# Performance work log

Measured on AMD Instinct MI355X. Metric: run time of the kernel, lower is better.

The kernel has to match this reference:

```python
import jax, jax.numpy as jnp
import numpy as np

B, N, C = 4, 4096, 256
H, D, K = 8, 32, 16  # heads, dim_head, knn


def setup_inputs() -> dict:
    key = jax.random.key(0)
    ks = jax.random.split(key, 7)
    s = 1.0 / np.sqrt(C)
    return {
        "x": jax.random.normal(ks[0], (B, N, C), dtype=jnp.float32),
        "Wq": jax.random.normal(ks[1], (C, H * D), dtype=jnp.float32) * s,
        "bq": jnp.zeros((H * D,), dtype=jnp.float32),
        "Wk": jax.random.normal(ks[2], (C, H * D), dtype=jnp.float32) * s,
        "bk": jnp.zeros((H * D,), dtype=jnp.float32),
        "Wv": jax.random.normal(ks[3], (C, H * D), dtype=jnp.float32) * s,
        "bv": jnp.zeros((H * D,), dtype=jnp.float32),
    }


def _knn_indices(x):
    # squared euclidean distances per batch: [B, N, N]
    sq = jnp.sum(x * x, axis=-1)
    d2 = sq[:, :, None] + sq[:, None, :] - 2.0 * jnp.einsum("bnc,bmc->bnm", x, x)
    # exclude self-loops (loop=False)
    eye = jnp.eye(x.shape[1], dtype=bool)
    d2 = jnp.where(eye[None], jnp.inf, d2)
    # k nearest neighbors (smallest distance)
    _, idx = jax.lax.top_k(-d2, K)  # [B, N, K]
    return idx


def reference(x, Wq, bq, Wk, bk, Wv, bv):
    idx = _knn_indices(x)  # [B, N, K] neighbor (source) node ids per target node
    # gather neighbor features: [B, N, K, C]
    xj = jax.vmap(lambda xb, ib: xb[ib])(x, idx)
    q = (x @ Wq + bq).reshape(B, N, H, D)           # target-node queries
    ke = (xj @ Wk + bk).reshape(B, N, K, H, D)      # per-edge keys
    ve = (xj @ Wv + bv).reshape(B, N, K, H, D)      # per-edge values
    scale = 1.0 / np.sqrt(D)
    scores = jnp.einsum("bnhd,bnkhd->bnkh", q, ke) * scale
    alpha = jax.nn.softmax(scores, axis=2)          # softmax over each node's K neighbors
    out = jnp.einsum("bnkh,bnkhd->bnhd", alpha, ve)
    return out.reshape(B, N, H * D)
```

## Files before the change

### kernel.cpp

```cpp
#include <hip/hip_runtime.h>
#include <cstdint>
#include <cstddef>

#define N_ 4096
#define C_ 256

typedef _Float16 h8 __attribute__((ext_vector_type(8)));
typedef _Float16 h4 __attribute__((ext_vector_type(4)));
typedef float f4 __attribute__((ext_vector_type(4)));

__device__ __forceinline__ void gl2lds16(const void* g, void* l) {
  __builtin_amdgcn_global_load_lds((const __attribute__((address_space(1))) void*)g,
                                   (__attribute__((address_space(3))) void*)l, 16, 0, 0);
}

__device__ __forceinline__ void ce_asc(double& a, double& b) {
  double mn = fmin(a, b), mx = fmax(a, b);
  a = mn; b = mx;
}

__device__ __forceinline__ void sort8_asc(double* c) {
  ce_asc(c[0], c[1]); ce_asc(c[2], c[3]); ce_asc(c[4], c[5]); ce_asc(c[6], c[7]);
  ce_asc(c[0], c[2]); ce_asc(c[1], c[3]); ce_asc(c[4], c[6]); ce_asc(c[5], c[7]);
  ce_asc(c[1], c[2]); ce_asc(c[5], c[6]);
  ce_asc(c[0], c[4]); ce_asc(c[1], c[5]); ce_asc(c[2], c[6]); ce_asc(c[3], c[7]);
  ce_asc(c[2], c[4]); ce_asc(c[3], c[5]);
  ce_asc(c[1], c[2]); ce_asc(c[3], c[4]); ce_asc(c[5], c[6]);
}

__device__ __forceinline__ void merge8_top16(double* karr, const double* c) {
#pragma unroll
  for (int i = 0; i < 8; i++)
    karr[8 + i] = fmin(karr[8 + i], c[7 - i]);
#pragma unroll
  for (int j = 8; j > 0; j >>= 1)
#pragma unroll
    for (int i = 0; i < 16; i++) {
      int l = i ^ j;
      if (l > i) ce_asc(karr[i], karr[l]);
    }
}

__global__ __launch_bounds__(256) void k_pre(const float* __restrict__ x,
                                             float* __restrict__ sq,
                                             _Float16* __restrict__ xh,
                                             _Float16* __restrict__ xl,
                                             const float* __restrict__ Wq,
                                             const float* __restrict__ Wk,
                                             const float* __restrict__ Wv,
                                             _Float16* __restrict__ wh,
                                             _Float16* __restrict__ wl) {
  int bid = blockIdx.x;
  if (bid < 4096) {
    int wave = threadIdx.x >> 6, lane = threadIdx.x & 63;
    int row = bid * 4 + wave;
    size_t off = (size_t)row * C_ + lane * 4;
    float4 v = *(const float4*)(x + off);
    h4 hi; hi[0] = (_Float16)v.x; hi[1] = (_Float16)v.y;
           hi[2] = (_Float16)v.z; hi[3] = (_Float16)v.w;
    h4 lo; lo[0] = (_Float16)(v.x - (float)hi[0]); lo[1] = (_Float16)(v.y - (float)hi[1]);
           lo[2] = (_Float16)(v.z - (float)hi[2]); lo[3] = (_Float16)(v.w - (float)hi[3]);
    *(h4*)(xh + off) = hi;
    *(h4*)(xl + off) = lo;
    float s = v.x * v.x + v.y * v.y + v.z * v.z + v.w * v.w;
    s += __shfl_xor(s, 32); s += __shfl_xor(s, 16); s += __shfl_xor(s, 8);
    s += __shfl_xor(s, 4);  s += __shfl_xor(s, 2);  s += __shfl_xor(s, 1);
    if (lane == 0) sq[row] = s;
  } else {
    int g = (bid - 4096) * 256 + threadIdx.x;
    int m = g >> 16, e = g & 65535;
    int k = e >> 8, j = e & 255;
    const float* W = (m == 0) ? Wq : ((m == 1) ? Wk : Wv);
    float v = W[k * 256 + j];
    _Float16 hi = (_Float16)v;
    _Float16 lo = (_Float16)(v - (float)hi);
    wh[m * 65536 + j * 256 + k] = hi;
    wl[m * 65536 + j * 256 + k] = lo;
  }
}

__global__ __launch_bounds__(256, 3) void k_proj(const _Float16* __restrict__ xh,
                                                 const _Float16* __restrict__ xl,
                                                 const _Float16* __restrict__ wh,
                                                 const _Float16* __restrict__ wl,
                                                 const float* __restrict__ bqp,
                                                 const float* __restrict__ bkp,
                                                 const float* __restrict__ bvp,
                                                 float* __restrict__ qf,
                                                 _Float16* __restrict__ kh,
                                                 _Float16* __restrict__ vh) {
  int tid = threadIdx.x;
  int bid = blockIdx.x;
  int m   = bid >> 8;
  int rb  = (bid >> 1) & 127;
  int cp  = bid & 1;
  int wave = tid >> 6, lane = tid & 63, quad = lane >> 4, l16 = lane & 15;
  const float* bb = (m == 0) ? bqp : ((m == 1) ? bkp : bvp);
  int row0 = rb * 128 + wave * 32;

  h8 Ah[2][8], Al[2][8];
#pragma unroll
  for (int rt = 0; rt < 2; rt++)
#pragma unroll
    for (int kc = 0; kc < 8; kc++) {
      size_t off = (size_t)(row0 + rt * 16 + l16) * C_ + kc * 32 + quad * 8;
      Ah[rt][kc] = *(const h8*)(xh + off);
      Al[rt][kc] = *(const h8*)(xl + off);
    }
  const _Float16* whm = wh + (size_t)m * 65536;
  const _Float16* wlm = wl + (size_t)m * 65536;

  f4 acc[2][8];
#pragma unroll
  for (int rt = 0; rt < 2; rt++)
#pragma unroll
    for (int ct = 0; ct < 8; ct++) acc[rt][ct] = f4{0.f, 0.f, 0.f, 0.f};
#pragma unroll
  for (int kc = 0; kc < 8; kc++) {
#pragma unroll
    for (int ct = 0; ct < 8; ct++) {
      int col = cp * 128 + ct * 16 + l16;
      h8 bh = *(const h8*)(whm + (size_t)col * 256 + kc * 32 + quad * 8);
      h8 bl = *(const h8*)(wlm + (size_t)col * 256 + kc * 32 + quad * 8);
#pragma unroll
      for (int rt = 0; rt < 2; rt++) {
        acc[rt][ct] = __builtin_amdgcn_mfma_f32_16x16x32_f16(Ah[rt][kc], bh, acc[rt][ct], 0, 0, 0);
        acc[rt][ct] = __builtin_amdgcn_mfma_f32_16x16x32_f16(Ah[rt][kc], bl, acc[rt][ct], 0, 0, 0);
        acc[rt][ct] = __builtin_amdgcn_mfma_f32_16x16x32_f16(Al[rt][kc], bh, acc[rt][ct], 0, 0, 0);
      }
    }
  }
  _Float16* d16 = (m == 1) ? kh : vh;
#pragma unroll
  for (int rt = 0; rt < 2; rt++)
#pragma unroll
    for (int ct = 0; ct < 8; ct++) {
      int col = cp * 128 + ct * 16 + l16;
      float bias = bb[col];
#pragma unroll
      for (int i = 0; i < 4; i++) {
        int r = row0 + rt * 16 + quad * 4 + i;
        float o = acc[rt][ct][i] + bias;
        if (m == 0) qf[(size_t)r * C_ + col] = o;
        else        d16[(size_t)r * C_ + col] = (_Float16)o;
      }
    }
}

__global__ __launch_bounds__(256, 2) void k_knn(const _Float16* __restrict__ xh,
                                                const _Float16* __restrict__ xl,
                                                const float* __restrict__ sq,
                                                double* __restrict__ pd) {
  __shared__ __align__(16) _Float16 Bh[16 * 528];
  __shared__ __align__(16) _Float16 Bl[16 * 528];
  __shared__ __align__(16) float sc[128 * 36];
  __shared__ float sqS[32];

  int tid = threadIdx.x;
  int wave = tid >> 6, lane = tid & 63, quad = lane >> 4, l16 = lane & 15;
  int bid = blockIdx.x;
  int s4 = bid & 3, tile = (bid >> 2) & 31, b = bid >> 7;
  int bN = b * N_, n0 = tile * 128, src0g = s4 * 1024;

  h8 Ah[2][8], Al[2][8];
  int tb = bN + n0 + wave * 32;
#pragma unroll
  for (int rt = 0; rt < 2; rt++)
#pragma unroll
    for (int kc = 0; kc < 8; kc++) {
      size_t off = (size_t)(tb + rt * 16 + l16) * C_ + kc * 32 + quad * 8;
      Ah[rt][kc] = *(const h8*)(xh + off);
      Al[rt][kc] = *(const h8*)(xl + off);
    }
  float sqT[2][4];
#pragma unroll
  for (int rt = 0; rt < 2; rt++)
#pragma unroll
    for (int i = 0; i < 4; i++)
      sqT[rt][i] = sq[tb + rt * 16 + quad * 4 + i];

  double karr[16];
#pragma unroll
  for (int p = 0; p < 16; p++) karr[p] = 1e300;
  int rowo = tid & 127, half = tid >> 7;

  {
    const _Float16* gh = xh + (size_t)(bN + src0g) * C_ + lane * 8;
    const _Float16* gl = xl + (size_t)(bN + src0g) * C_ + lane * 8;
#pragma unroll
    for (int k = 0; k < 4; k++) {
      int seg = wave * 4 + k;
      gl2lds16(gh + seg * 512, &Bh[seg * 528]);
      gl2lds16(gl + seg * 512, &Bl[seg * 528]);
    }
    if (tid < 32) sqS[tid] = sq[bN + src0g + tid];
  }

  int hb0 = ((l16 >> 1) * 528) + ((l16 & 1) * 256) + quad * 8;
  int hb1 = (((16 + l16) >> 1) * 528) + ((l16 & 1) * 256) + quad * 8;

#pragma unroll 1
  for (int ch = 0; ch < 32; ch++) {
    int src0 = src0g + ch * 32;
    __syncthreads();

    f4 acc[2][2];
#pragma unroll
    for (int rt = 0; rt < 2; rt++)
#pragma unroll
      for (int ct = 0; ct < 2; ct++) acc[rt][ct] = f4{0.f, 0.f, 0.f, 0.f};
#pragma unroll
    for (int kc = 0; kc < 8; kc++) {
      h8 bh0 = *(const h8*)(&Bh[hb0 + kc * 32]);
      h8 bh1 = *(const h8*)(&Bh[hb1 + kc * 32]);
      h8 bl0 = *(const h8*)(&Bl[hb0 + kc * 32]);
      h8 bl1 = *(const h8*)(&Bl[hb1 + kc * 32]);
#pragma unroll
      for (int rt = 0; rt < 2; rt++) {
        acc[rt][0] = __builtin_amdgcn_mfma_f32_16x16x32_f16(Ah[rt][kc], bh0, acc[rt][0], 0, 0, 0);
        acc[rt][0] = __builtin_amdgcn_mfma_f32_16x16x32_f16(Ah[rt][kc], bl0, acc[rt][0], 0, 0, 0);
        acc[rt][0] = __builtin_amdgcn_mfma_f32_16x16x32_f16(Al[rt][kc], bh0, acc[rt][0], 0, 0, 0);
        acc[rt][1] = __builtin_amdgcn_mfma_f32_16x16x32_f16(Ah[rt][kc], bh1, acc[rt][1], 0, 0, 0);
        acc[rt][1] = __builtin_amdgcn_mfma_f32_16x16x32_f16(Ah[rt][kc], bl1, acc[rt][1], 0, 0, 0);
        acc[rt][1] = __builtin_amdgcn_mfma_f32_16x16x32_f16(Al[rt][kc], bh1, acc[rt][1], 0, 0, 0);
      }
    }
    float sqSr[2] = {sqS[l16], sqS[16 + l16]};
#pragma unroll
    for (int rt = 0; rt < 2; rt++)
#pragma unroll
      for (int ct = 0; ct < 2; ct++) {
        int c = ct * 16 + l16;
#pragma unroll
        for (int i = 0; i < 4; i++) {
          int r = wave * 32 + rt * 16 + quad * 4 + i;
          float d2 = sqT[rt][i] + sqSr[ct] - 2.0f * acc[rt][ct][i];
          if (n0 + r == src0 + c) d2 = 1e38f;
          sc[r * 36 + c] = d2;
        }
      }
    __syncthreads();

    if (ch < 31) {
      int srcn = src0 + 32;
      const _Float16* gh = xh + (size_t)(bN + srcn) * C_ + lane * 8;
      const _Float16* gl = xl + (size_t)(bN + srcn) * C_ + lane * 8;
#pragma unroll
      for (int k = 0; k < 4; k++) {
        int seg = wave * 4 + k;
        gl2lds16(gh + seg * 512, &Bh[seg * 528]);
        gl2lds16(gl + seg * 512, &Bl[seg * 528]);
      }
      if (tid < 32) sqS[tid] = sq[bN + srcn + tid];
    }

#pragma unroll
    for (int bt = 0; bt < 2; bt++) {
      float dv[8];
#pragma unroll
      for (int k4 = 0; k4 < 2; k4++)
        *(float4*)&dv[k4 * 4] = *(const float4*)(&sc[rowo * 36 + half * 16 + bt * 8 + k4 * 4]);
      double c8[8];
#pragma unroll
      for (int j = 0; j < 8; j++) {
        double key = (double)dv[j];
        c8[j] = __longlong_as_double(__double_as_longlong(key) |
                                     (unsigned)(src0 + half * 16 + bt * 8 + j));
      }
      sort8_asc(c8);
      merge8_top16(karr, c8);
    }
  }

  __syncthreads();
  double* scd = (double*)sc;
  if (tid >= 128) {
#pragma unroll
    for (int p = 0; p < 16; p++) scd[(tid - 128) * 17 + p] = karr[p];
  }
  __syncthreads();
  if (tid < 128) {
#pragma unroll
    for (int i = 0; i < 16; i++)
      karr[i] = fmin(karr[i], scd[tid * 17 + (15 - i)]);
#pragma unroll
    for (int j = 8; j > 0; j >>= 1)
#pragma unroll
      for (int i = 0; i < 16; i++) {
        int l = i ^ j;
        if (l > i) ce_asc(karr[i], karr[l]);
      }
#pragma unroll
    for (int p = 0; p < 16; p++)
      pd[((size_t)bid * 128 + tid) * 16 + p] = karr[p];
  }
}

__global__ __launch_bounds__(256) void k_attn(const float* __restrict__ qf,
                                              const _Float16* __restrict__ kh,
                                              const _Float16* __restrict__ vh,
                                              const double* __restrict__ pd,
                                              float* __restrict__ out) {
  int wave = threadIdx.x >> 6, lane = threadIdx.x & 63;
  int g = blockIdx.x * 4 + wave;
  int bN = (g >> 12) << 12;
  int el = lane & 15;

  int b = g >> 12, n = g & 4095;
  int tile = n >> 7, r = n & 127;
  size_t pbase = (size_t)(((b * 32 + tile) * 4) * 128 + r) * 16;
  double a = pd[pbase + el];
#pragma unroll
  for (int s = 1; s < 4; s++) {
    double bb = pd[pbase + (size_t)s * 128 * 16 + el];
    double br = __shfl(bb, (lane & ~15) | (15 - el));
    a = fmin(a, br);
#pragma unroll
    for (int j = 8; j > 0; j >>= 1) {
      double o = __shfl(a, lane ^ j);
      a = (el & j) ? fmax(a, o) : fmin(a, o);
    }
  }
  int my = (int)(__double_as_longlong(a) & 0xFFF);

  float4 q4 = *(const float4*)(qf + (size_t)g * C_ + lane * 4);
  const float scale = 0.17677669529663687f;

  float s[16];
  h4 vv[16];
#pragma unroll
  for (int j = 0; j < 16; j++) {
    int nb = __shfl(my, j);
    size_t base = (size_t)(bN + nb) * C_ + lane * 4;
    h4 k4 = *(const h4*)(kh + base);
    vv[j] = *(const h4*)(vh + base);
    float p = (float)k4[0] * q4.x + (float)k4[1] * q4.y +
              (float)k4[2] * q4.z + (float)k4[3] * q4.w;
    p += __shfl_xor(p, 1); p += __shfl_xor(p, 2); p += __shfl_xor(p, 4);
    s[j] = p * scale;
  }
  float mx = s[0];
#pragma unroll
  for (int j = 1; j < 16; j++) mx = fmaxf(mx, s[j]);
  float den = 0.f;
#pragma unroll
  for (int j = 0; j < 16; j++) { s[j] = __expf(s[j] - mx); den += s[j]; }
  float inv = 1.0f / den;
  float4 o; o.x = 0.f; o.y = 0.f; o.z = 0.f; o.w = 0.f;
#pragma unroll
  for (int j = 0; j < 16; j++) {
    float w = s[j] * inv;
    o.x = fmaf(w, (float)vv[j][0], o.x); o.y = fmaf(w, (float)vv[j][1], o.y);
    o.z = fmaf(w, (float)vv[j][2], o.z); o.w = fmaf(w, (float)vv[j][3], o.w);
  }
  *(float4*)(out + (size_t)g * C_ + lane * 4) = o;
}

extern "C" void kernel_launch(void* const* d_in, const int* in_sizes, int n_in,
                              void* d_out, int out_size, void* d_ws, size_t ws_size,
                              hipStream_t stream) {
  const float* x  = (const float*)d_in[0];
  const float* Wq = (const float*)d_in[1];
  const float* bq = (const float*)d_in[2];
  const float* Wk = (const float*)d_in[3];
  const float* bk = (const float*)d_in[4];
  const float* Wv = (const float*)d_in[5];
  const float* bv = (const float*)d_in[6];
  float* out = (float*)d_out;

  char* ws = (char*)d_ws;
  float*     sqp  = (float*)(ws + 0);
  _Float16*  xh   = (_Float16*)(ws + 65536);
  _Float16*  xl   = (_Float16*)(ws + 8454144);
  float*     qf   = (float*)(ws + 16842752);
  _Float16*  khp  = (_Float16*)(ws + 33619968);
  _Float16*  vhp  = (_Float16*)(ws + 50397184);
  double*    pd   = (double*)(ws + 67174400);
  _Float16*  whf  = (_Float16*)(ws + 76611584);
  _Float16*  wlf  = (_Float16*)(ws + 77004800);

  k_pre   <<<4864, 256, 0, stream>>>(x, sqp, xh, xl, Wq, Wk, Wv, whf, wlf);
  k_proj  <<<768,  256, 0, stream>>>(xh, xl, whf, wlf, bq, bk, bv, qf, khp, vhp);
  k_knn   <<<512,  256, 0, stream>>>(xh, xl, sqp, pd);
  k_attn  <<<4096, 256, 0, stream>>>(qf, khp, vhp, pd, out);
}
```

Measured before the change: 284.9 us.

## Interleave K and V into one buffer and drop low-part weight MFMA for K/V

K and V projections are written into a single interleaved fp16 buffer, so each neighbor gather in the attention kernel becomes one 16-byte load instead of two 8-byte loads from separate arrays. For the K and V projections, the weight low-part correction MFMA is dropped, cutting MFMA count and weight loads by a third for those blocks. The Q path keeps the three-term split. This reduces K/V precision slightly, and the interleaved stores in the projection are scattered 2-byte writes.

```diff
diff --git a/kernel.cpp b/kernel.cpp
--- a/kernel.cpp
+++ b/kernel.cpp
@@ -87,8 +87,7 @@
                                                  const float* __restrict__ bkp,
                                                  const float* __restrict__ bvp,
                                                  float* __restrict__ qf,
-                                                 _Float16* __restrict__ kh,
-                                                 _Float16* __restrict__ vh) {
+                                                 _Float16* __restrict__ kv) {
   int tid = threadIdx.x;
   int bid = blockIdx.x;
   int m   = bid >> 8;
@@ -108,43 +107,71 @@
       Al[rt][kc] = *(const h8*)(xl + off);
     }
   const _Float16* whm = wh + (size_t)m * 65536;
-  const _Float16* wlm = wl + (size_t)m * 65536;
 
   f4 acc[2][8];
 #pragma unroll
   for (int rt = 0; rt < 2; rt++)
 #pragma unroll
     for (int ct = 0; ct < 8; ct++) acc[rt][ct] = f4{0.f, 0.f, 0.f, 0.f};
-#pragma unroll
-  for (int kc = 0; kc < 8; kc++) {
-#pragma unroll
-    for (int ct = 0; ct < 8; ct++) {
-      int col = cp * 128 + ct * 16 + l16;
-      h8 bh = *(const h8*)(whm + (size_t)col * 256 + kc * 32 + quad * 8);
-      h8 bl = *(const h8*)(wlm + (size_t)col * 256 + kc * 32 + quad * 8);
-#pragma unroll
-      for (int rt = 0; rt < 2; rt++) {
-        acc[rt][ct] = __builtin_amdgcn_mfma_f32_16x16x32_f16(Ah[rt][kc], bh, acc[rt][ct], 0, 0, 0);
-        acc[rt][ct] = __builtin_amdgcn_mfma_f32_16x16x32_f16(Ah[rt][kc], bl, acc[rt][ct], 0, 0, 0);
-        acc[rt][ct] = __builtin_amdgcn_mfma_f32_16x16x32_f16(Al[rt][kc], bh, acc[rt][ct], 0, 0, 0);
-      }
-    }
-  }
-  _Float16* d16 = (m == 1) ? kh : vh;
-#pragma unroll
-  for (int rt = 0; rt < 2; rt++)
-#pragma unroll
-    for (int ct = 0; ct < 8; ct++) {
-      int col = cp * 128 + ct * 16 + l16;
-      float bias = bb[col];
-#pragma unroll
-      for (int i = 0; i < 4; i++) {
-        int r = row0 + rt * 16 + quad * 4 + i;
-        float o = acc[rt][ct][i] + bias;
-        if (m == 0) qf[(size_t)r * C_ + col] = o;
-        else        d16[(size_t)r * C_ + col] = (_Float16)o;
-      }
-    }
+
+  if (m == 0) {
+    const _Float16* wlm = wl;
+#pragma unroll
+    for (int kc = 0; kc < 8; kc++) {
+#pragma unroll
+      for (int ct = 0; ct < 8; ct++) {
+        int col = cp * 128 + ct * 16 + l16;
+        h8 bh = *(const h8*)(whm + (size_t)col * 256 + kc * 32 + quad * 8);
+        h8 bl = *(const h8*)(wlm + (size_t)col * 256 + kc * 32 + quad * 8);
+#pragma unroll
+        for (int rt = 0; rt < 2; rt++) {
+          acc[rt][ct] = __builtin_amdgcn_mfma_f32_16x16x32_f16(Ah[rt][kc], bh, acc[rt][ct], 0, 0, 0);
+          acc[rt][ct] = __builtin_amdgcn_mfma_f32_16x16x32_f16(Ah[rt][kc], bl, acc[rt][ct], 0, 0, 0);
+          acc[rt][ct] = __builtin_amdgcn_mfma_f32_16x16x32_f16(Al[rt][kc], bh, acc[rt][ct], 0, 0, 0);
+        }
+      }
+    }
+#pragma unroll
+    for (int rt = 0; rt < 2; rt++)
+#pragma unroll
+      for (int ct = 0; ct < 8; ct++) {
+        int col = cp * 128 + ct * 16 + l16;
+        float bias = bb[col];
+#pragma unroll
+        for (int i = 0; i < 4; i++) {
+          int r = row0 + rt * 16 + quad * 4 + i;
+          qf[(size_t)r * C_ + col] = acc[rt][ct][i] + bias;
+        }
+      }
+  } else {
+#pragma unroll
+    for (int kc = 0; kc < 8; kc++) {
+#pragma unroll
+      for (int ct = 0; ct < 8; ct++) {
+        int col = cp * 128 + ct * 16 + l16;
+        h8 bh = *(const h8*)(whm + (size_t)col * 256 + kc * 32 + quad * 8);
+#pragma unroll
+        for (int rt = 0; rt < 2; rt++) {
+          acc[rt][ct] = __builtin_amdgcn_mfma_f32_16x16x32_f16(Ah[rt][kc], bh, acc[rt][ct], 0, 0, 0);
+          acc[rt][ct] = __builtin_amdgcn_mfma_f32_16x16x32_f16(Al[rt][kc], bh, acc[rt][ct], 0, 0, 0);
+        }
+      }
+    }
+    int voff = (m == 1) ? 0 : 4;
+#pragma unroll
+    for (int rt = 0; rt < 2; rt++)
+#pragma unroll
+      for (int ct = 0; ct < 8; ct++) {
+        int col = cp * 128 + ct * 16 + l16;
+        float bias = bb[col];
+#pragma unroll
+        for (int i = 0; i < 4; i++) {
+          int r = row0 + rt * 16 + quad * 4 + i;
+          float o = acc[rt][ct][i] + bias;
+          kv[(size_t)r * 512 + ((col >> 2) * 8) + voff + (col & 3)] = (_Float16)o;
+        }
+      }
+  }
 }
 
 __global__ __launch_bounds__(256, 2) void k_knn(const _Float16* __restrict__ xh,
@@ -297,8 +324,7 @@
 }
 
 __global__ __launch_bounds__(256) void k_attn(const float* __restrict__ qf,
-                                              const _Float16* __restrict__ kh,
-                                              const _Float16* __restrict__ vh,
+                                              const _Float16* __restrict__ kvp,
                                               const double* __restrict__ pd,
                                               float* __restrict__ out) {
   int wave = threadIdx.x >> 6, lane = threadIdx.x & 63;
@@ -331,11 +357,12 @@
 #pragma unroll
   for (int j = 0; j < 16; j++) {
     int nb = __shfl(my, j);
-    size_t base = (size_t)(bN + nb) * C_ + lane * 4;
-    h4 k4 = *(const h4*)(kh + base);
-    vv[j] = *(const h4*)(vh + base);
-    float p = (float)k4[0] * q4.x + (float)k4[1] * q4.y +
-              (float)k4[2] * q4.z + (float)k4[3] * q4.w;
+    size_t base = (size_t)(bN + nb) * 512 + lane * 8;
+    h8 kv8 = *(const h8*)(kvp + base);
+    float p = (float)kv8[0] * q4.x + (float)kv8[1] * q4.y +
+              (float)kv8[2] * q4.z + (float)kv8[3] * q4.w;
+    h4 v4; v4[0] = kv8[4]; v4[1] = kv8[5]; v4[2] = kv8[6]; v4[3] = kv8[7];
+    vv[j] = v4;
     p += __shfl_xor(p, 1); p += __shfl_xor(p, 2); p += __shfl_xor(p, 4);
     s[j] = p * scale;
   }
@@ -373,14 +400,13 @@
   _Float16*  xh   = (_Float16*)(ws + 65536);
   _Float16*  xl   = (_Float16*)(ws + 8454144);
   float*     qf   = (float*)(ws + 16842752);
-  _Float16*  khp  = (_Float16*)(ws + 33619968);
-  _Float16*  vhp  = (_Float16*)(ws + 50397184);
+  _Float16*  kvp  = (_Float16*)(ws + 33619968);
   double*    pd   = (double*)(ws + 67174400);
   _Float16*  whf  = (_Float16*)(ws + 76611584);
   _Float16*  wlf  = (_Float16*)(ws + 77004800);
 
   k_pre   <<<4864, 256, 0, stream>>>(x, sqp, xh, xl, Wq, Wk, Wv, whf, wlf);
-  k_proj  <<<768,  256, 0, stream>>>(xh, xl, whf, wlf, bq, bk, bv, qf, khp, vhp);
+  k_proj  <<<768,  256, 0, stream>>>(xh, xl, whf, wlf, bq, bk, bv, qf, kvp);
   k_knn   <<<512,  256, 0, stream>>>(xh, xl, sqp, pd);
-  k_attn  <<<4096, 256, 0, stream>>>(qf, khp, vhp, pd, out);
-}
+  k_attn  <<<4096, 256, 0, stream>>>(qf, kvp, pd, out);
+}
```

After: 288.5 us. Within noise of the previous version (+1.3%).
